# Kernel tuning notes

Hardware: AMD Instinct MI355X
Metric: run time of the kernel (lower is better)

The kernel has to match this reference:

```python
import jax, jax.numpy as jnp
import numpy as np

N, D, H, L, GHD, OUT = 512, 128, 4, 4, 32, 128  # nodes, input_dim, heads, layers, graph_hidden_dim, output_dim


def _xavier(key, shape):
    fan_in, fan_out = shape[0], shape[1]
    limit = float(np.sqrt(6.0 / (fan_in + fan_out)))
    return jax.random.uniform(key, shape, jnp.float32, -limit, limit)


def setup_inputs() -> dict:
    key = jax.random.key(0)
    ks = jax.random.split(key, 16)
    node_feat = jax.random.normal(ks[0], (N, D), jnp.float32)
    edge_feat = jax.random.normal(ks[1], (N, N, D), jnp.float32)
    adj = jax.random.uniform(ks[2], (H, N, N), jnp.float32)
    # per-(head,layer) edge weights: all [D, GHD]
    W_edge = _xavier(ks[3], (D, GHD))[None, None] * jnp.ones((H, L, 1, 1), jnp.float32)
    W_edge = jax.random.uniform(ks[3], (H, L, D, GHD), jnp.float32, -0.1, 0.1)
    # per-layer node weights (input dim grows by GHD each layer): [H, D + l*GHD, GHD]
    Wn0 = _xavier(ks[4], (D + 0 * GHD, GHD))[None] * jnp.ones((H, 1, 1), jnp.float32)
    Wn0 = jax.random.uniform(ks[4], (H, D + 0 * GHD, GHD), jnp.float32, -0.1, 0.1)
    Wn1 = jax.random.uniform(ks[5], (H, D + 1 * GHD, GHD), jnp.float32, -0.1, 0.1)
    Wn2 = jax.random.uniform(ks[6], (H, D + 2 * GHD, GHD), jnp.float32, -0.1, 0.1)
    Wn3 = jax.random.uniform(ks[7], (H, D + 3 * GHD, GHD), jnp.float32, -0.1, 0.1)
    # final linear: in = hidden_dim * head_num = L*GHD*H = 512, out = OUT
    W_lin = _xavier(ks[8], (L * GHD * H, OUT))
    b_lin = jnp.zeros((OUT,), jnp.float32)
    return {"node_feat": node_feat, "edge_feat": edge_feat, "adj": adj,
            "W_edge": W_edge, "Wn0": Wn0, "Wn1": Wn1, "Wn2": Wn2, "Wn3": Wn3,
            "W_lin": W_lin, "b_lin": b_lin}


def reference(node_feat, edge_feat, adj, W_edge, Wn0, Wn1, Wn2, Wn3, W_lin, b_lin):
    # mean over second node axis; einsum('ijk,kp->ijp') then mean(dim=1) == mean then matmul
    edge_mean = jnp.mean(edge_feat, axis=1)  # [N, D]
    Wn = [Wn0, Wn1, Wn2, Wn3]
    head_feats = []
    for h in range(H):
        A = adj[h]                         # [N, N]
        deg = jnp.sum(A, axis=1)           # [N]
        denom = (deg + (deg == 0).astype(deg.dtype))[:, None]  # zero-degree -> divide by 1
        outputs = node_feat
        cache = [node_feat]
        outs = []
        for l in range(L):
            e_out = edge_mean @ W_edge[h, l]            # [N, GHD]
            n_out = A @ (outputs @ Wn[l][h])            # chain_matmul(A, X, W)
            g = jax.nn.relu((e_out + n_out) / denom)    # [N, GHD]
            cache.append(g)
            outputs = jnp.concatenate(cache, axis=-1)
            outs.append(g)                              # dropout is eval-mode identity
        head_feats.append(jnp.concatenate(outs, axis=-1) + node_feat)  # [N, D]
    all_heads = jnp.concatenate(head_feats, axis=-1)    # [N, H*D]
    return all_heads @ W_lin + b_lin                    # [N, OUT]
```

## Files before the change

kernel.cpp:

```cpp
#include <hip/hip_runtime.h>
#include <cstddef>

#define NN 512
#define DD 128
#define HH 4
#define LL 4
#define GHD 32
#define OUTD 128

static constexpr size_t OFF_EM  = 0;
static constexpr size_t OFF_ANF = OFF_EM  + (size_t)NN * DD;
static constexpr size_t OFF_DEN = OFF_ANF + (size_t)HH * NN * DD;
static constexpr size_t OFF_G   = OFF_DEN + (size_t)HH * NN;
static constexpr size_t OFF_AG  = OFF_G   + (size_t)HH * LL * NN * GHD;

__global__ __launch_bounds__(256) void prep_kernel(
    const float* __restrict__ node_feat,
    const float* __restrict__ edge_feat,
    const float* __restrict__ adj,
    float* __restrict__ ws)
{
    const int t = threadIdx.x;
    const int b = blockIdx.x;

    __shared__ float4 red[256];
    __shared__ float  Arow[8][NN + 4];
    __shared__ float  dred[8][33];

    if (b < NN) {
        const int q = t & 31;
        const int g = t >> 5;
        const float4* ef = reinterpret_cast<const float4*>(edge_feat)
                         + (size_t)b * NN * (DD / 4);
        float4 acc; acc.x = acc.y = acc.z = acc.w = 0.f;
        #pragma unroll 4
        for (int j = g; j < NN; j += 8) {
            float4 v = ef[(size_t)j * (DD / 4) + q];
            acc.x += v.x; acc.y += v.y; acc.z += v.z; acc.w += v.w;
        }
        red[t] = acc;
        __syncthreads();
        for (int s = 128; s >= 32; s >>= 1) {
            if (t < s) {
                float4 o = red[t + s], m = red[t];
                m.x += o.x; m.y += o.y; m.z += o.z; m.w += o.w;
                red[t] = m;
            }
            __syncthreads();
        }
        if (t < 32) {
            const float inv = 1.0f / (float)NN;
            float4 m = red[t];
            m.x *= inv; m.y *= inv; m.z *= inv; m.w *= inv;
            reinterpret_cast<float4*>(ws + OFF_EM + (size_t)b * DD)[t] = m;
        }
    } else {
        const int bb = b - NN;
        const int h  = bb >> 6;
        const int r0 = (bb & 63) * 8;
        const float* A = adj + (size_t)h * NN * NN;

        for (int idx = t; idx < 8 * NN; idx += 256) {
            int rr = idx >> 9;
            int jj = idx & (NN - 1);
            Arow[rr][jj] = A[(size_t)(r0 + rr) * NN + jj];
        }
        __syncthreads();

        {
            const int rr = t >> 5, lane = t & 31;
            float s = 0.f;
            for (int j = lane; j < NN; j += 32) s += Arow[rr][j];
            dred[rr][lane] = s;
            __syncthreads();
            if (t < 8) {
                float d = 0.f;
                #pragma unroll 8
                for (int j = 0; j < 32; ++j) d += dred[t][j];
                ws[OFF_DEN + (size_t)h * NN + r0 + t] = d + (d == 0.f ? 1.f : 0.f);
            }
        }

        const int c  = t & 127;
        const int rb = t >> 7;
        float a0 = 0.f, a1 = 0.f, a2 = 0.f, a3 = 0.f;
        #pragma unroll 4
        for (int j = 0; j < NN; ++j) {
            float nf = node_feat[(size_t)j * DD + c];
            a0 += Arow[rb + 0][j] * nf;
            a1 += Arow[rb + 2][j] * nf;
            a2 += Arow[rb + 4][j] * nf;
            a3 += Arow[rb + 6][j] * nf;
        }
        float* anf = ws + OFF_ANF + ((size_t)h * NN + r0) * DD;
        anf[(rb + 0) * DD + c] = a0;
        anf[(rb + 2) * DD + c] = a1;
        anf[(rb + 4) * DD + c] = a2;
        anf[(rb + 6) * DD + c] = a3;
    }
}

template <int LAYER>
__global__ __launch_bounds__(256) void layer_kernel(
    const float* __restrict__ adj,
    const float* __restrict__ W_edge,
    const float* __restrict__ Wn,
    float* __restrict__ ws)
{
    constexpr int KIN = DD + GHD * LAYER;
    const int b  = blockIdx.x;
    const int h  = b >> 6;
    const int r0 = (b & 63) * 8;
    const int t  = threadIdx.x;
    const int rr = t >> 5;
    const int r  = r0 + rr;
    const int c  = t & 31;

    const float* em  = ws + OFF_EM;
    const float* anf = ws + OFF_ANF;
    const float* den = ws + OFF_DEN;
    float* G  = ws + OFF_G;
    float* AG = ws + OFF_AG;

    __shared__ float agl[8][GHD];

    if (LAYER > 0) {
        const float4* A4 = reinterpret_cast<const float4*>(
            adj + ((size_t)h * NN + r) * NN);
        const float* gp = G + (((size_t)h * LL + (LAYER - 1)) * NN) * GHD;
        float s0 = 0.f, s1 = 0.f, s2 = 0.f, s3 = 0.f;
        #pragma unroll 4
        for (int j4 = 0; j4 < NN / 4; ++j4) {
            float4 a = A4[j4];
            const float* gpj = gp + (size_t)j4 * 4 * GHD + c;
            s0 += a.x * gpj[0 * GHD];
            s1 += a.y * gpj[1 * GHD];
            s2 += a.z * gpj[2 * GHD];
            s3 += a.w * gpj[3 * GHD];
        }
        float ag = (s0 + s1) + (s2 + s3);
        agl[rr][c] = ag;
        AG[(((size_t)h * 3 + (LAYER - 1)) * NN + r) * GHD + c] = ag;
    }
    __syncthreads();

    float acc = 0.f;
    {
        const float* We  = W_edge + (((size_t)h * LL + LAYER) * DD) * GHD;
        const float4* e4 = reinterpret_cast<const float4*>(em + (size_t)r * DD);
        #pragma unroll 4
        for (int k4 = 0; k4 < DD / 4; ++k4) {
            float4 e = e4[k4];
            const float* w = We + (size_t)k4 * 4 * GHD + c;
            acc += e.x * w[0 * GHD] + e.y * w[1 * GHD]
                 + e.z * w[2 * GHD] + e.w * w[3 * GHD];
        }
    }
    {
        const float* Wnl = Wn + (size_t)h * KIN * GHD;
        const float4* a4 = reinterpret_cast<const float4*>(
            anf + ((size_t)h * NN + r) * DD);
        #pragma unroll 4
        for (int k4 = 0; k4 < DD / 4; ++k4) {
            float4 e = a4[k4];
            const float* w = Wnl + (size_t)k4 * 4 * GHD + c;
            acc += e.x * w[0 * GHD] + e.y * w[1 * GHD]
                 + e.z * w[2 * GHD] + e.w * w[3 * GHD];
        }
        #pragma unroll
        for (int kk = 0; kk < LAYER; ++kk) {
            const float* w = Wnl + (size_t)(DD + kk * GHD) * GHD + c;
            if (kk == LAYER - 1) {
                #pragma unroll 8
                for (int m = 0; m < GHD; ++m) acc += agl[rr][m] * w[m * GHD];
            } else {
                const float* agk = AG + (((size_t)h * 3 + kk) * NN + r) * GHD;
                #pragma unroll 8
                for (int m = 0; m < GHD; ++m) acc += agk[m] * w[m * GHD];
            }
        }
    }

    float dn = den[(size_t)h * NN + r];
    float gv = acc / dn;
    gv = gv > 0.f ? gv : 0.f;
    G[(((size_t)h * LL + LAYER) * NN + r) * GHD + c] = gv;
}

__global__ __launch_bounds__(256) void final_kernel(
    const float* __restrict__ node_feat,
    const float* __restrict__ W_lin,
    const float* __restrict__ b_lin,
    const float* __restrict__ ws,
    float* __restrict__ out)
{
    const int b = blockIdx.x;
    const int t = threadIdx.x;
    const int n = b * 2 + (t >> 7);
    const int o = t & 127;
    const float* G   = ws + OFF_G;
    const float* nfr = node_feat + (size_t)n * DD;

    float acc = b_lin[o];
    #pragma unroll
    for (int h = 0; h < HH; ++h) {
        #pragma unroll
        for (int l = 0; l < LL; ++l) {
            const float* gr = G + (((size_t)h * LL + l) * NN + n) * GHD;
            const float* w  = W_lin + (size_t)(h * DD + l * GHD) * OUTD + o;
            #pragma unroll 8
            for (int cc = 0; cc < GHD; ++cc) {
                float ah = gr[cc] + nfr[l * GHD + cc];
                acc += ah * w[(size_t)cc * OUTD];
            }
        }
    }
    out[(size_t)n * OUTD + o] = acc;
}

extern "C" void kernel_launch(void* const* d_in, const int* in_sizes, int n_in,
                              void* d_out, int out_size, void* d_ws, size_t ws_size,
                              hipStream_t stream)
{
    const float* node_feat = (const float*)d_in[0];
    const float* edge_feat = (const float*)d_in[1];
    const float* adj       = (const float*)d_in[2];
    const float* W_edge    = (const float*)d_in[3];
    const float* Wn0       = (const float*)d_in[4];
    const float* Wn1       = (const float*)d_in[5];
    const float* Wn2       = (const float*)d_in[6];
    const float* Wn3       = (const float*)d_in[7];
    const float* W_lin     = (const float*)d_in[8];
    const float* b_lin     = (const float*)d_in[9];
    float* out = (float*)d_out;
    float* ws  = (float*)d_ws;

    hipLaunchKernelGGL(prep_kernel, dim3(NN + HH * 64), dim3(256), 0, stream,
                       node_feat, edge_feat, adj, ws);
    hipLaunchKernelGGL(layer_kernel<0>, dim3(HH * 64), dim3(256), 0, stream,
                       adj, W_edge, Wn0, ws);
    hipLaunchKernelGGL(layer_kernel<1>, dim3(HH * 64), dim3(256), 0, stream,
                       adj, W_edge, Wn1, ws);
    hipLaunchKernelGGL(layer_kernel<2>, dim3(HH * 64), dim3(256), 0, stream,
                       adj, W_edge, Wn2, ws);
    hipLaunchKernelGGL(layer_kernel<3>, dim3(HH * 64), dim3(256), 0, stream,
                       adj, W_edge, Wn3, ws);
    hipLaunchKernelGGL(final_kernel, dim3(NN / 2), dim3(256), 0, stream,
                       node_feat, W_lin, b_lin, ws, out);
}
```

Before: 363.4 us.

## Split reductions across more blocks and hoist edge projection into separate kernel

Spreads the edge-mean reduction over four blocks per row, each writing a partial sum. The edge projection for every head and layer now runs in a new kernel instead of inside each layer kernel. Layer and final kernels split their K-dimension across warps with shared-memory reductions, and the prep adjacency work uses four rows per block, so all stages launch many more blocks. The goal is to fill the GPU with work, since the earlier kernels ran only 256 to 768 blocks. The cost is extra workspace traffic, partial-sum passes and one more launch.

```diff
diff --git a/kernel.cpp b/kernel.cpp
--- a/kernel.cpp
+++ b/kernel.cpp
@@ -8,10 +8,11 @@
 #define GHD 32
 #define OUTD 128
 
-static constexpr size_t OFF_EM  = 0;
-static constexpr size_t OFF_ANF = OFF_EM  + (size_t)NN * DD;
+static constexpr size_t OFF_EP  = 0;
+static constexpr size_t OFF_ANF = OFF_EP  + (size_t)4 * NN * DD;
 static constexpr size_t OFF_DEN = OFF_ANF + (size_t)HH * NN * DD;
-static constexpr size_t OFF_G   = OFF_DEN + (size_t)HH * NN;
+static constexpr size_t OFF_EO  = OFF_DEN + (size_t)HH * NN;
+static constexpr size_t OFF_G   = OFF_EO  + (size_t)HH * LL * NN * GHD;
 static constexpr size_t OFF_AG  = OFF_G   + (size_t)HH * LL * NN * GHD;
 
 __global__ __launch_bounds__(256) void prep_kernel(
@@ -22,22 +23,23 @@
 {
     const int t = threadIdx.x;
     const int b = blockIdx.x;
-
-    __shared__ float4 red[256];
-    __shared__ float  Arow[8][NN + 4];
-    __shared__ float  dred[8][33];
-
-    if (b < NN) {
-        const int q = t & 31;
-        const int g = t >> 5;
+    __shared__ __align__(16) float smem[4 * NN + 256];
+
+    if (b >= 512) {
+        const int bb = b - 512;
+        const int r  = bb >> 2;
+        const int jq = bb & 3;
+        const int q  = t & 31;
+        const int g  = t >> 5;
         const float4* ef = reinterpret_cast<const float4*>(edge_feat)
-                         + (size_t)b * NN * (DD / 4);
+                         + ((size_t)r * NN + (size_t)jq * 128) * (DD / 4);
         float4 acc; acc.x = acc.y = acc.z = acc.w = 0.f;
-        #pragma unroll 4
-        for (int j = g; j < NN; j += 8) {
-            float4 v = ef[(size_t)j * (DD / 4) + q];
+        #pragma unroll
+        for (int k = 0; k < 16; ++k) {
+            float4 v = ef[(size_t)(g + 8 * k) * (DD / 4) + q];
             acc.x += v.x; acc.y += v.y; acc.z += v.z; acc.w += v.w;
         }
+        float4* red = reinterpret_cast<float4*>(smem);
         red[t] = acc;
         __syncthreads();
         for (int s = 128; s >= 32; s >>= 1) {
@@ -48,143 +50,161 @@
             }
             __syncthreads();
         }
-        if (t < 32) {
-            const float inv = 1.0f / (float)NN;
-            float4 m = red[t];
-            m.x *= inv; m.y *= inv; m.z *= inv; m.w *= inv;
-            reinterpret_cast<float4*>(ws + OFF_EM + (size_t)b * DD)[t] = m;
-        }
+        if (t < 32)
+            reinterpret_cast<float4*>(ws + OFF_EP + ((size_t)jq * NN + r) * DD)[t] = red[t];
     } else {
-        const int bb = b - NN;
-        const int h  = bb >> 6;
-        const int r0 = (bb & 63) * 8;
+        const int h  = b >> 7;
+        const int r0 = (b & 127) * 4;
         const float* A = adj + (size_t)h * NN * NN;
-
-        for (int idx = t; idx < 8 * NN; idx += 256) {
-            int rr = idx >> 9;
-            int jj = idx & (NN - 1);
-            Arow[rr][jj] = A[(size_t)(r0 + rr) * NN + jj];
-        }
+        float* Arow = smem;
+        float* dred = smem + 4 * NN;
+
+        for (int idx = t; idx < 4 * NN; idx += 256)
+            Arow[idx] = A[(size_t)r0 * NN + idx];
         __syncthreads();
 
         {
-            const int rr = t >> 5, lane = t & 31;
+            const int rr = t >> 6, lane = t & 63;
             float s = 0.f;
-            for (int j = lane; j < NN; j += 32) s += Arow[rr][j];
-            dred[rr][lane] = s;
+            #pragma unroll 8
+            for (int j = lane; j < NN; j += 64) s += Arow[rr * NN + j];
+            dred[t] = s;
             __syncthreads();
-            if (t < 8) {
+            if (t < 4) {
                 float d = 0.f;
-                #pragma unroll 8
-                for (int j = 0; j < 32; ++j) d += dred[t][j];
+                for (int j = 0; j < 64; ++j) d += dred[t * 64 + j];
                 ws[OFF_DEN + (size_t)h * NN + r0 + t] = d + (d == 0.f ? 1.f : 0.f);
             }
         }
 
         const int c  = t & 127;
         const int rb = t >> 7;
-        float a0 = 0.f, a1 = 0.f, a2 = 0.f, a3 = 0.f;
+        float a0 = 0.f, a1 = 0.f;
         #pragma unroll 4
         for (int j = 0; j < NN; ++j) {
             float nf = node_feat[(size_t)j * DD + c];
-            a0 += Arow[rb + 0][j] * nf;
-            a1 += Arow[rb + 2][j] * nf;
-            a2 += Arow[rb + 4][j] * nf;
-            a3 += Arow[rb + 6][j] * nf;
+            a0 += Arow[(rb + 0) * NN + j] * nf;
+            a1 += Arow[(rb + 2) * NN + j] * nf;
         }
         float* anf = ws + OFF_ANF + ((size_t)h * NN + r0) * DD;
         anf[(rb + 0) * DD + c] = a0;
         anf[(rb + 2) * DD + c] = a1;
-        anf[(rb + 4) * DD + c] = a2;
-        anf[(rb + 6) * DD + c] = a3;
-    }
-}
-
-template <int LAYER>
+    }
+}
+
+__global__ __launch_bounds__(256) void eout_kernel(
+    const float* __restrict__ W_edge,
+    float* __restrict__ ws)
+{
+    const int b  = blockIdx.x;
+    const int rg = b & 31;
+    const int hl = b >> 5;
+    const int r0 = rg * 16;
+    const int t  = threadIdx.x;
+    __shared__ float em[16 * DD];
+
+    const float* P = ws + OFF_EP;
+    for (int idx = t; idx < 16 * DD; idx += 256) {
+        int r = r0 + (idx >> 7), k = idx & 127;
+        size_t o = (size_t)r * DD + k;
+        em[idx] = (P[o] + P[(size_t)NN * DD + o]
+                 + P[2 * (size_t)NN * DD + o] + P[3 * (size_t)NN * DD + o])
+                * (1.0f / (float)NN);
+    }
+    __syncthreads();
+
+    const int c  = t & 31;
+    const int rr = t >> 5;
+    const float* We = W_edge + (size_t)hl * DD * GHD;
+    float s0 = 0.f, s1 = 0.f;
+    #pragma unroll 4
+    for (int k = 0; k < DD; ++k) {
+        float w = We[(size_t)k * GHD + c];
+        s0 += em[rr * DD + k] * w;
+        s1 += em[(rr + 8) * DD + k] * w;
+    }
+    float* eo = ws + OFF_EO + ((size_t)hl * NN + r0) * GHD;
+    eo[(size_t)rr * GHD + c]       = s0;
+    eo[(size_t)(rr + 8) * GHD + c] = s1;
+}
+
+template <int L>
 __global__ __launch_bounds__(256) void layer_kernel(
     const float* __restrict__ adj,
-    const float* __restrict__ W_edge,
     const float* __restrict__ Wn,
     float* __restrict__ ws)
 {
-    constexpr int KIN = DD + GHD * LAYER;
-    const int b  = blockIdx.x;
-    const int h  = b >> 6;
-    const int r0 = (b & 63) * 8;
-    const int t  = threadIdx.x;
-    const int rr = t >> 5;
-    const int r  = r0 + rr;
-    const int c  = t & 31;
-
-    const float* em  = ws + OFF_EM;
+    constexpr int KIN = DD + GHD * L;
+    const int b   = blockIdx.x;
+    const int h   = b >> 8;
+    const int r0  = (b & 255) * 2;
+    const int t   = threadIdx.x;
+    const int rr  = t >> 7;
+    const int sub = (t >> 5) & 3;
+    const int c   = t & 31;
+    const int r   = r0 + rr;
+
     const float* anf = ws + OFF_ANF;
     const float* den = ws + OFF_DEN;
+    const float* eo  = ws + OFF_EO;
     float* G  = ws + OFF_G;
     float* AG = ws + OFF_AG;
 
-    __shared__ float agl[8][GHD];
-
-    if (LAYER > 0) {
+    __shared__ float smem[256 + 64 + 256];
+    float* agp = smem;
+    float* agl = smem + 256;
+    float* pp  = smem + 320;
+
+    if (L > 0) {
         const float4* A4 = reinterpret_cast<const float4*>(
             adj + ((size_t)h * NN + r) * NN);
-        const float* gp = G + (((size_t)h * LL + (LAYER - 1)) * NN) * GHD;
-        float s0 = 0.f, s1 = 0.f, s2 = 0.f, s3 = 0.f;
+        const float* gp = G + (((size_t)h * LL + (L - 1)) * NN) * GHD;
+        float s = 0.f;
         #pragma unroll 4
-        for (int j4 = 0; j4 < NN / 4; ++j4) {
+        for (int j4 = sub * 32; j4 < sub * 32 + 32; ++j4) {
             float4 a = A4[j4];
-            const float* gpj = gp + (size_t)j4 * 4 * GHD + c;
-            s0 += a.x * gpj[0 * GHD];
-            s1 += a.y * gpj[1 * GHD];
-            s2 += a.z * gpj[2 * GHD];
-            s3 += a.w * gpj[3 * GHD];
-        }
-        float ag = (s0 + s1) + (s2 + s3);
-        agl[rr][c] = ag;
-        AG[(((size_t)h * 3 + (LAYER - 1)) * NN + r) * GHD + c] = ag;
-    }
-    __syncthreads();
-
-    float acc = 0.f;
-    {
-        const float* We  = W_edge + (((size_t)h * LL + LAYER) * DD) * GHD;
-        const float4* e4 = reinterpret_cast<const float4*>(em + (size_t)r * DD);
-        #pragma unroll 4
-        for (int k4 = 0; k4 < DD / 4; ++k4) {
-            float4 e = e4[k4];
-            const float* w = We + (size_t)k4 * 4 * GHD + c;
-            acc += e.x * w[0 * GHD] + e.y * w[1 * GHD]
-                 + e.z * w[2 * GHD] + e.w * w[3 * GHD];
-        }
-    }
+            const float* gj = gp + (size_t)j4 * 4 * GHD + c;
+            s += a.x * gj[0] + a.y * gj[GHD] + a.z * gj[2 * GHD] + a.w * gj[3 * GHD];
+        }
+        agp[t] = s;
+    }
+    __syncthreads();
+    if (L > 0 && sub == 0) {
+        float ag = agp[rr * 128 + c] + agp[rr * 128 + 32 + c]
+                 + agp[rr * 128 + 64 + c] + agp[rr * 128 + 96 + c];
+        AG[(((size_t)h * 3 + (L - 1)) * NN + r) * GHD + c] = ag;
+        agl[rr * GHD + c] = ag;
+    }
+    __syncthreads();
+
+    float p = 0.f;
     {
         const float* Wnl = Wn + (size_t)h * KIN * GHD;
-        const float4* a4 = reinterpret_cast<const float4*>(
-            anf + ((size_t)h * NN + r) * DD);
-        #pragma unroll 4
-        for (int k4 = 0; k4 < DD / 4; ++k4) {
-            float4 e = a4[k4];
-            const float* w = Wnl + (size_t)k4 * 4 * GHD + c;
-            acc += e.x * w[0 * GHD] + e.y * w[1 * GHD]
-                 + e.z * w[2 * GHD] + e.w * w[3 * GHD];
-        }
-        #pragma unroll
-        for (int kk = 0; kk < LAYER; ++kk) {
-            const float* w = Wnl + (size_t)(DD + kk * GHD) * GHD + c;
-            if (kk == LAYER - 1) {
-                #pragma unroll 8
-                for (int m = 0; m < GHD; ++m) acc += agl[rr][m] * w[m * GHD];
-            } else {
-                const float* agk = AG + (((size_t)h * 3 + kk) * NN + r) * GHD;
-                #pragma unroll 8
-                for (int m = 0; m < GHD; ++m) acc += agk[m] * w[m * GHD];
-            }
-        }
-    }
-
-    float dn = den[(size_t)h * NN + r];
-    float gv = acc / dn;
-    gv = gv > 0.f ? gv : 0.f;
-    G[(((size_t)h * LL + LAYER) * NN + r) * GHD + c] = gv;
+        const float* ar  = anf + ((size_t)h * NN + r) * DD;
+        #pragma unroll 8
+        for (int k = sub * 32; k < sub * 32 + 32; ++k)
+            p += ar[k] * Wnl[(size_t)k * GHD + c];
+        if (sub < L) {
+            const float* agk = (sub == L - 1)
+                ? (agl + rr * GHD)
+                : (AG + (((size_t)h * 3 + sub) * NN + r) * GHD);
+            const float* w = Wnl + (size_t)(DD + sub * GHD) * GHD + c;
+            #pragma unroll 8
+            for (int m = 0; m < GHD; ++m)
+                p += agk[m] * w[(size_t)m * GHD];
+        }
+    }
+    pp[t] = p;
+    __syncthreads();
+    if (sub == 0) {
+        float tot = pp[rr * 128 + c] + pp[rr * 128 + 32 + c]
+                  + pp[rr * 128 + 64 + c] + pp[rr * 128 + 96 + c]
+                  + eo[(((size_t)h * LL + L) * NN + r) * GHD + c];
+        float dn = den[(size_t)h * NN + r];
+        float gv = tot / dn;
+        gv = gv > 0.f ? gv : 0.f;
+        G[(((size_t)h * LL + L) * NN + r) * GHD + c] = gv;
+    }
 }
 
 __global__ __launch_bounds__(256) void final_kernel(
@@ -194,28 +214,31 @@
     const float* __restrict__ ws,
     float* __restrict__ out)
 {
-    const int b = blockIdx.x;
-    const int t = threadIdx.x;
-    const int n = b * 2 + (t >> 7);
-    const int o = t & 127;
-    const float* G   = ws + OFF_G;
-    const float* nfr = node_feat + (size_t)n * DD;
-
-    float acc = b_lin[o];
+    const int b  = blockIdx.x;
+    const int n  = b >> 1;
+    const int oh = b & 1;
+    const int t  = threadIdx.x;
+    const int ol = t & 63;
+    const int ks = t >> 6;
+    const int o  = oh * 64 + ol;
+    const float* G = ws + OFF_G;
+    __shared__ float red[256];
+
+    float p = 0.f;
     #pragma unroll
-    for (int h = 0; h < HH; ++h) {
-        #pragma unroll
-        for (int l = 0; l < LL; ++l) {
-            const float* gr = G + (((size_t)h * LL + l) * NN + n) * GHD;
-            const float* w  = W_lin + (size_t)(h * DD + l * GHD) * OUTD + o;
-            #pragma unroll 8
-            for (int cc = 0; cc < GHD; ++cc) {
-                float ah = gr[cc] + nfr[l * GHD + cc];
-                acc += ah * w[(size_t)cc * OUTD];
-            }
-        }
-    }
-    out[(size_t)n * OUTD + o] = acc;
+    for (int l = 0; l < LL; ++l) {
+        const float* gr  = G + (((size_t)ks * LL + l) * NN + n) * GHD;
+        const float* nfr = node_feat + (size_t)n * DD + l * GHD;
+        const float* w   = W_lin + (size_t)(ks * DD + l * GHD) * OUTD + o;
+        #pragma unroll 8
+        for (int cc = 0; cc < GHD; ++cc)
+            p += (gr[cc] + nfr[cc]) * w[(size_t)cc * OUTD];
+    }
+    red[t] = p;
+    __syncthreads();
+    if (ks == 0)
+        out[(size_t)n * OUTD + o] =
+            red[ol] + red[64 + ol] + red[128 + ol] + red[192 + ol] + b_lin[o];
 }
 
 extern "C" void kernel_launch(void* const* d_in, const int* in_sizes, int n_in,
@@ -235,16 +258,13 @@
     float* out = (float*)d_out;
     float* ws  = (float*)d_ws;
 
-    hipLaunchKernelGGL(prep_kernel, dim3(NN + HH * 64), dim3(256), 0, stream,
+    hipLaunchKernelGGL(prep_kernel, dim3(512 + 2048), dim3(256), 0, stream,
                        node_feat, edge_feat, adj, ws);
-    hipLaunchKernelGGL(layer_kernel<0>, dim3(HH * 64), dim3(256), 0, stream,
-                       adj, W_edge, Wn0, ws);
-    hipLaunchKernelGGL(layer_kernel<1>, dim3(HH * 64), dim3(256), 0, stream,
-                       adj, W_edge, Wn1, ws);
-    hipLaunchKernelGGL(layer_kernel<2>, dim3(HH * 64), dim3(256), 0, stream,
-                       adj, W_edge, Wn2, ws);
-    hipLaunchKernelGGL(layer_kernel<3>, dim3(HH * 64), dim3(256), 0, stream,
-                       adj, W_edge, Wn3, ws);
-    hipLaunchKernelGGL(final_kernel, dim3(NN / 2), dim3(256), 0, stream,
+    hipLaunchKernelGGL(eout_kernel, dim3(512), dim3(256), 0, stream, W_edge, ws);
+    hipLaunchKernelGGL(layer_kernel<0>, dim3(1024), dim3(256), 0, stream, adj, Wn0, ws);
+    hipLaunchKernelGGL(layer_kernel<1>, dim3(1024), dim3(256), 0, stream, adj, Wn1, ws);
+    hipLaunchKernelGGL(layer_kernel<2>, dim3(1024), dim3(256), 0, stream, adj, Wn2, ws);
+    hipLaunchKernelGGL(layer_kernel<3>, dim3(1024), dim3(256), 0, stream, adj, Wn3, ws);
+    hipLaunchKernelGGL(final_kernel, dim3(1024), dim3(256), 0, stream,
                        node_feat, W_lin, b_lin, ws, out);
 }
```

Measured after the change: 330.8 us. 9.0% less time.
